# Kernel optimization log

Measured on AMD Instinct MI355X. Metric: run time of the kernel, lower is better.

Reference implementation:

```python
import jax, jax.numpy as jnp
import numpy as np


def setup_inputs() -> dict:
    key = jax.random.key(0)
    k1, k2, k3 = jax.random.split(key, 3)
    L, B, T, H = 2, 16, 512, 12
    NUM_CUT = 1            # cuts per feature -> D+1 = 2 bins
    NUM_LEAF = (NUM_CUT + 1) ** H  # 4096
    NUM_CLASSES = 1000
    x = jax.random.normal(k1, (L, B, T, H), dtype=jnp.float32)
    cuts = jax.random.uniform(k2, (H, NUM_CUT), dtype=jnp.float32)
    leaf_score = jax.random.uniform(k3, (NUM_LEAF, NUM_CLASSES), dtype=jnp.float32)
    return {"x": x, "cuts": cuts, "leaf_score": leaf_score}


def reference(x, cuts, leaf_score):
    # Faithful to source: torch_bin RETURNS h (pre-softmax logits); temperature unused.
    xl = x[-1]                      # [B, T, H] -- only the last layer is used
    B, T, H = xl.shape
    D = cuts.shape[1]
    W = jnp.linspace(1.0, D + 1.0, D + 1).astype(xl.dtype)          # [D+1]
    sorted_cuts = jnp.sort(cuts, axis=-1)                            # [H, D]
    b = jnp.cumsum(
        jnp.concatenate([jnp.zeros((H, 1), dtype=xl.dtype), -sorted_cuts], axis=1),
        axis=1,
    )                                                                # [H, D+1]
    # h[b,t,f,:] = x[b,t,f] * W + b[f]  (outer product per scalar feature)
    h = xl[..., None] * W + b                                        # [B, T, H, D+1]
    # kron-product reduce over features -> leaf weights [B, T, (D+1)^H]
    leaf = h[..., 0, :]
    for i in range(1, H):
        leaf = (leaf[..., :, None] * h[..., i, None, :]).reshape(B, T, -1)
    out = jnp.einsum('btl,lc->btc', leaf, leaf_score)                # [B, T, C]
    return jnp.mean(out, axis=1)                                     # [B, C]
```

## Files before the change

kernel.cpp:

```cpp
#include <hip/hip_runtime.h>

#define HF 12
#define NLEAF 4096
#define NB 16
#define NT 512
#define NC 1000
#define NTC 8
#define TCH 64
#define TSUB 16
#define NSUB (TCH / TSUB)
#define LCH 64
#define NLCH (NLEAF / LCH)
#define NCT 4
#define INVT (1.0f / 512.0f)

__global__ __launch_bounds__(256) void k1_leaf(const float* __restrict__ x,
                                               const float* __restrict__ cuts,
                                               float* __restrict__ Sp) {
  const int blk = blockIdx.x;
  const int tid = threadIdx.x;

  __shared__ float h0s[TSUB][HF], h1s[TSUB][HF];
  __shared__ float Phis[TSUB][64], Plos[TSUB][64];

  const float* xb = x + (size_t)NB * NT * HF + (size_t)blk * (TCH * HF);

  const int  tl  = tid / HF;
  const int  f   = tid - tl * HF;
  const bool ldr = (tid < TSUB * HF);
  const float cf = ldr ? cuts[f] : 0.f;
  float xv = ldr ? xb[tid] : 0.f;

  float acc[16];
#pragma unroll
  for (int k = 0; k < 16; ++k) acc[k] = 0.f;

  const int w  = tid >> 6;
  const int lo = tid & 63;

  for (int ts = 0; ts < NSUB; ++ts) {
    if (ldr) {
      h0s[tl][f] = xv;
      h1s[tl][f] = 2.f * xv - cf;
    }
    __syncthreads();
    if (ldr && ts + 1 < NSUB) xv = xb[(ts + 1) * TSUB * HF + tid];

#pragma unroll
    for (int r = 0; r < 8; ++r) {
      const int task = r * 256 + tid;
      const int t2   = task >> 7;
      const int half = (task >> 6) & 1;
      const int idx  = task & 63;
      const float* hh0 = h0s[t2];
      const float* hh1 = h1s[t2];
      float p = 1.f;
#pragma unroll
      for (int i = 0; i < 6; ++i) {
        const int ff  = half * 6 + i;
        const int bit = (idx >> (5 - i)) & 1;
        p *= bit ? hh1[ff] : hh0[ff];
      }
      if (half) Plos[t2][idx] = p;
      else      Phis[t2][(idx & 3) * 16 + (idx >> 2)] = p;
    }
    __syncthreads();

#pragma unroll
    for (int t2 = 0; t2 < TSUB; ++t2) {
      const float  plo = Plos[t2][lo];
      const float4* ph = (const float4*)&Phis[t2][w * 16];
      const float4 p0 = ph[0], p1 = ph[1], p2 = ph[2], p3 = ph[3];
      acc[0]  += p0.x * plo;  acc[1]  += p0.y * plo;
      acc[2]  += p0.z * plo;  acc[3]  += p0.w * plo;
      acc[4]  += p1.x * plo;  acc[5]  += p1.y * plo;
      acc[6]  += p1.z * plo;  acc[7]  += p1.w * plo;
      acc[8]  += p2.x * plo;  acc[9]  += p2.y * plo;
      acc[10] += p2.z * plo;  acc[11] += p2.w * plo;
      acc[12] += p3.x * plo;  acc[13] += p3.y * plo;
      acc[14] += p3.z * plo;  acc[15] += p3.w * plo;
    }
  }

  float* sp = Sp + (size_t)blk * NLEAF;
#pragma unroll
  for (int k = 0; k < 16; ++k) sp[k * 256 + tid] = acc[k];
}

__global__ __launch_bounds__(256) void k2f(const float* __restrict__ Sp,
                                           const float* __restrict__ score,
                                           float* __restrict__ out) {
  const int lc  = blockIdx.x / NCT;
  const int ct  = blockIdx.x % NCT;
  const int tid = threadIdx.x;

  __shared__ float Stl[NB][LCH];

  for (int i = tid; i < NB * LCH; i += 256) {
    const int b  = i >> 6;
    const int ll = i & 63;
    const float* sp = Sp + (size_t)(b * NTC) * NLEAF + lc * LCH + ll;
    float v = 0.f;
#pragma unroll
    for (int tc = 0; tc < NTC; ++tc) v += sp[(size_t)tc * NLEAF];
    Stl[b][ll] = v * INVT;
  }
  __syncthreads();

  const int c = ct * 256 + tid;
  if (c < NC) {
    float acc[NB];
#pragma unroll
    for (int b = 0; b < NB; ++b) acc[b] = 0.f;

    const float* sc = score + (size_t)(lc * LCH) * NC + c;
    for (int l0 = 0; l0 < LCH; l0 += 8) {
      float sv[8];
#pragma unroll
      for (int j = 0; j < 8; ++j) sv[j] = sc[(size_t)(l0 + j) * NC];
#pragma unroll
      for (int b = 0; b < NB; ++b) {
        const float4* r = (const float4*)&Stl[b][l0];
        const float4 r0 = r[0], r1 = r[1];
        acc[b] += r0.x * sv[0] + r0.y * sv[1] + r0.z * sv[2] + r0.w * sv[3]
                + r1.x * sv[4] + r1.y * sv[5] + r1.z * sv[6] + r1.w * sv[7];
      }
    }
#pragma unroll
    for (int b = 0; b < NB; ++b)
      atomicAdd(&out[b * NC + c], acc[b]);
  }
}

extern "C" void kernel_launch(void* const* d_in, const int* in_sizes, int n_in,
                              void* d_out, int out_size, void* d_ws, size_t ws_size,
                              hipStream_t stream) {
  const float* x     = (const float*)d_in[0];
  const float* cuts  = (const float*)d_in[1];
  const float* score = (const float*)d_in[2];
  float* out = (float*)d_out;

  float* Sp = (float*)d_ws;

  hipMemsetAsync(out, 0, (size_t)NB * NC * sizeof(float), stream);
  k1_leaf<<<NB * NTC, 256, 0, stream>>>(x, cuts, Sp);
  k2f<<<NLCH * NCT, 256, 0, stream>>>(Sp, score, out);
}
```

Baseline: 85.25 us.

## Fuse memset, leaf kernel and score GEMV into one cooperative kernel with grid sync

Combines the output memset, the leaf-weight accumulation kernel and the leaf-score contraction into a single cooperative launch of 256 blocks. Blocks 0-127 compute partial leaf sums while the remaining blocks zero the output, then a grid-wide barrier precedes the contraction phase. This removes two extra launches and the gaps between them, but adds grid-sync cost and relies on all 256 blocks being co-resident.

After: 128.2 us. 1.5x slower.

```diff
diff --git a/kernel.cpp b/kernel.cpp
--- a/kernel.cpp
+++ b/kernel.cpp
@@ -1,4 +1,7 @@
 #include <hip/hip_runtime.h>
+#include <hip/hip_cooperative_groups.h>
+
+namespace cg = cooperative_groups;
 
 #define HF 12
 #define NLEAF 4096
@@ -13,88 +16,91 @@
 #define NLCH (NLEAF / LCH)
 #define NCT 4
 #define INVT (1.0f / 512.0f)
+#define NBLK 256
 
-__global__ __launch_bounds__(256) void k1_leaf(const float* __restrict__ x,
-                                               const float* __restrict__ cuts,
-                                               float* __restrict__ Sp) {
+__global__ __launch_bounds__(256) void ndt_fused(
+    const float* __restrict__ x, const float* __restrict__ cuts,
+    const float* __restrict__ score, float* __restrict__ Sp,
+    float* __restrict__ out) {
   const int blk = blockIdx.x;
   const int tid = threadIdx.x;
 
   __shared__ float h0s[TSUB][HF], h1s[TSUB][HF];
   __shared__ float Phis[TSUB][64], Plos[TSUB][64];
+  __shared__ float Stl[NB][LCH];
 
-  const float* xb = x + (size_t)NB * NT * HF + (size_t)blk * (TCH * HF);
+  if (blk < NB * NTC) {
+    const float* xb = x + (size_t)NB * NT * HF + (size_t)blk * (TCH * HF);
 
-  const int  tl  = tid / HF;
-  const int  f   = tid - tl * HF;
-  const bool ldr = (tid < TSUB * HF);
-  const float cf = ldr ? cuts[f] : 0.f;
-  float xv = ldr ? xb[tid] : 0.f;
+    const int  tl  = tid / HF;
+    const int  f   = tid - tl * HF;
+    const bool ldr = (tid < TSUB * HF);
+    const float cf = ldr ? cuts[f] : 0.f;
+    float xv = ldr ? xb[tid] : 0.f;
 
-  float acc[16];
+    float acc[16];
 #pragma unroll
-  for (int k = 0; k < 16; ++k) acc[k] = 0.f;
+    for (int k = 0; k < 16; ++k) acc[k] = 0.f;
 
-  const int w  = tid >> 6;
-  const int lo = tid & 63;
+    const int w  = tid >> 6;
+    const int lo = tid & 63;
 
-  for (int ts = 0; ts < NSUB; ++ts) {
-    if (ldr) {
-      h0s[tl][f] = xv;
-      h1s[tl][f] = 2.f * xv - cf;
-    }
-    __syncthreads();
-    if (ldr && ts + 1 < NSUB) xv = xb[(ts + 1) * TSUB * HF + tid];
+    for (int ts = 0; ts < NSUB; ++ts) {
+      if (ldr) {
+        h0s[tl][f] = xv;
+        h1s[tl][f] = 2.f * xv - cf;
+      }
+      __syncthreads();
+      if (ldr && ts + 1 < NSUB) xv = xb[(ts + 1) * TSUB * HF + tid];
 
 #pragma unroll
-    for (int r = 0; r < 8; ++r) {
-      const int task = r * 256 + tid;
-      const int t2   = task >> 7;
-      const int half = (task >> 6) & 1;
-      const int idx  = task & 63;
-      const float* hh0 = h0s[t2];
-      const float* hh1 = h1s[t2];
-      float p = 1.f;
+      for (int r = 0; r < 8; ++r) {
+        const int task = r * 256 + tid;
+        const int t2   = task >> 7;
+        const int half = (task >> 6) & 1;
+        const int idx  = task & 63;
+        const float* hh0 = h0s[t2];
+        const float* hh1 = h1s[t2];
+        float p = 1.f;
 #pragma unroll
-      for (int i = 0; i < 6; ++i) {
-        const int ff  = half * 6 + i;
-        const int bit = (idx >> (5 - i)) & 1;
-        p *= bit ? hh1[ff] : hh0[ff];
+        for (int i = 0; i < 6; ++i) {
+          const int ff  = half * 6 + i;
+          const int bit = (idx >> (5 - i)) & 1;
+          p *= bit ? hh1[ff] : hh0[ff];
+        }
+        if (half) Plos[t2][idx] = p;
+        else      Phis[t2][(idx & 3) * 16 + (idx >> 2)] = p;
       }
-      if (half) Plos[t2][idx] = p;
-      else      Phis[t2][(idx & 3) * 16 + (idx >> 2)] = p;
-    }
-    __syncthreads();
+      __syncthreads();
 
 #pragma unroll
-    for (int t2 = 0; t2 < TSUB; ++t2) {
-      const float  plo = Plos[t2][lo];
-      const float4* ph = (const float4*)&Phis[t2][w * 16];
-      const float4 p0 = ph[0], p1 = ph[1], p2 = ph[2], p3 = ph[3];
-      acc[0]  += p0.x * plo;  acc[1]  += p0.y * plo;
-      acc[2]  += p0.z * plo;  acc[3]  += p0.w * plo;
-      acc[4]  += p1.x * plo;  acc[5]  += p1.y * plo;
-      acc[6]  += p1.z * plo;  acc[7]  += p1.w * plo;
-      acc[8]  += p2.x * plo;  acc[9]  += p2.y * plo;
-      acc[10] += p2.z * plo;  acc[11] += p2.w * plo;
-      acc[12] += p3.x * plo;  acc[13] += p3.y * plo;
-      acc[14] += p3.z * plo;  acc[15] += p3.w * plo;
+      for (int t2 = 0; t2 < TSUB; ++t2) {
+        const float  plo = Plos[t2][lo];
+        const float4* ph = (const float4*)&Phis[t2][w * 16];
+        const float4 p0 = ph[0], p1 = ph[1], p2 = ph[2], p3 = ph[3];
+        acc[0]  += p0.x * plo;  acc[1]  += p0.y * plo;
+        acc[2]  += p0.z * plo;  acc[3]  += p0.w * plo;
+        acc[4]  += p1.x * plo;  acc[5]  += p1.y * plo;
+        acc[6]  += p1.z * plo;  acc[7]  += p1.w * plo;
+        acc[8]  += p2.x * plo;  acc[9]  += p2.y * plo;
+        acc[10] += p2.z * plo;  acc[11] += p2.w * plo;
+        acc[12] += p3.x * plo;  acc[13] += p3.y * plo;
+        acc[14] += p3.z * plo;  acc[15] += p3.w * plo;
+      }
     }
+
+    float* sp = Sp + (size_t)blk * NLEAF;
+#pragma unroll
+    for (int k = 0; k < 16; ++k) sp[k * 256 + tid] = acc[k];
+  } else {
+    const int i = (blk - NB * NTC) * 256 + tid;
+    if (i < NB * NC) out[i] = 0.f;
   }
 
-  float* sp = Sp + (size_t)blk * NLEAF;
-#pragma unroll
-  for (int k = 0; k < 16; ++k) sp[k * 256 + tid] = acc[k];
-}
+  cg::this_grid().sync();
 
-__global__ __launch_bounds__(256) void k2f(const float* __restrict__ Sp,
-                                           const float* __restrict__ score,
-                                           float* __restrict__ out) {
-  const int lc  = blockIdx.x / NCT;
-  const int ct  = blockIdx.x % NCT;
-  const int tid = threadIdx.x;
-
-  __shared__ float Stl[NB][LCH];
+  const int lc = blk / NCT;
+  const int ct = blk % NCT;
 
   for (int i = tid; i < NB * LCH; i += 256) {
     const int b  = i >> 6;
@@ -109,9 +115,9 @@
 
   const int c = ct * 256 + tid;
   if (c < NC) {
-    float acc[NB];
+    float acc2[NB];
 #pragma unroll
-    for (int b = 0; b < NB; ++b) acc[b] = 0.f;
+    for (int b = 0; b < NB; ++b) acc2[b] = 0.f;
 
     const float* sc = score + (size_t)(lc * LCH) * NC + c;
     for (int l0 = 0; l0 < LCH; l0 += 8) {
@@ -122,13 +128,13 @@
       for (int b = 0; b < NB; ++b) {
         const float4* r = (const float4*)&Stl[b][l0];
         const float4 r0 = r[0], r1 = r[1];
-        acc[b] += r0.x * sv[0] + r0.y * sv[1] + r0.z * sv[2] + r0.w * sv[3]
-                + r1.x * sv[4] + r1.y * sv[5] + r1.z * sv[6] + r1.w * sv[7];
+        acc2[b] += r0.x * sv[0] + r0.y * sv[1] + r0.z * sv[2] + r0.w * sv[3]
+                 + r1.x * sv[4] + r1.y * sv[5] + r1.z * sv[6] + r1.w * sv[7];
       }
     }
 #pragma unroll
     for (int b = 0; b < NB; ++b)
-      atomicAdd(&out[b * NC + c], acc[b]);
+      atomicAdd(&out[b * NC + c], acc2[b]);
   }
 }
 
@@ -139,10 +145,9 @@
   const float* cuts  = (const float*)d_in[1];
   const float* score = (const float*)d_in[2];
   float* out = (float*)d_out;
+  float* Sp  = (float*)d_ws;
 
-  float* Sp = (float*)d_ws;
-
-  hipMemsetAsync(out, 0, (size_t)NB * NC * sizeof(float), stream);
-  k1_leaf<<<NB * NTC, 256, 0, stream>>>(x, cuts, Sp);
-  k2f<<<NLCH * NCT, 256, 0, stream>>>(Sp, score, out);
+  void* args[] = {(void*)&x, (void*)&cuts, (void*)&score, (void*)&Sp, (void*)&out};
+  hipLaunchCooperativeKernel((const void*)ndt_fused, dim3(NBLK), dim3(256),
+                             args, 0, stream);
 }
```
